# Performance work log

Measured on AMD Instinct MI355X. Metric: run time of the kernel, lower is better.

## Reference

```python
import jax, jax.numpy as jnp
import numpy as np

K = 7
PAD = K // 2
SIG_L = (4.0, 6.0, 8.0)
SIG_S = (1.0, 2.0, 3.0)
DORD = (0, 1, 2)
ANG = (1, 2, 3, 4)
N_INV, N_EQ, N_CP = 8, 16, 16
LN_EPS = 1e-5


def _polar_grid(k):
    c = jnp.arange(k, dtype=jnp.float32) - (k - 1) / 2.0
    gy, gx = jnp.meshgrid(c, c, indexing='ij')
    r = jnp.sqrt(gx * gx + gy * gy + 1e-8)
    th = jnp.arctan2(gy, gx)
    return r, th


def _gaussian_basis(r, sigmas, orders, n):
    # Gaussian-derivative radial basis (Eqs. 13-14): cycle over (order, sigma) combos.
    combos = [(s, d) for d in orders for s in sigmas]
    mats = []
    for i in range(n):
        s, d = combos[i % len(combos)]
        u = r / s
        g = jnp.exp(-0.5 * u * u)
        p = jnp.ones_like(u) if d == 0 else (u if d == 1 else u * u - 1.0)
        psi = p * g
        mats.append(psi / jnp.sqrt(jnp.sum(psi * psi) + 1e-8))
    return jnp.stack(mats)  # [n, K, K]


def _harmonic_basis(r, th, w1, b1, w2, b2, n):
    # Circular harmonics (Eqs. 15-16): learnable radial MLP x cos/sin(n*theta).
    kk = r.size
    rad = jnp.tanh(r.reshape(kk, 1) @ w1 + b1) @ w2 + b2  # [K*K, M]
    tf = th.reshape(kk)
    ang = jnp.stack([f(o * tf) for o in ANG for f in (jnp.cos, jnp.sin)])  # [2L, K*K]
    basis = (rad.T[:, None, :] * ang[None, :, :]).reshape(-1, K, K)  # [M*2L, K, K]
    return basis[:n]


def _coeff(z, w1, b1, w2, b2, n, cout):
    h = jax.nn.relu(z @ w1 + b1)
    return (h @ w2 + b2).reshape(z.shape[0], n, cout)  # [B, N, C_out]


def _pconv(feature, kernel):
    # Per-sample kernel shared across input channels: conv2d with weight
    # expand over C_in == conv of the channel-sum with the per-(b,o) kernel.
    B, Cin, H, W = feature.shape
    Cout = kernel.shape[1]
    fs = feature.sum(axis=1)[None]  # [1, B, H, W]
    rhs = kernel.reshape(B * Cout, 1, K, K)
    out = jax.lax.conv_general_dilated(fs, rhs, (1, 1), [(PAD, PAD), (PAD, PAD)], feature_group_count=B)
    return out.reshape(B, Cout, H, W)


def _ln_c(x, g, b):
    # LayerNorm over channel dim (permute(0,2,3,1) -> LN -> permute back)
    mu = jnp.mean(x, axis=1, keepdims=True)
    var = jnp.var(x, axis=1, keepdims=True)
    return (x - mu) * jax.lax.rsqrt(var + LN_EPS) * g[None, :, None, None] + b[None, :, None, None]


def setup_inputs() -> dict:
    key = jax.random.key(0)
    ks = jax.random.split(key, 16)
    B, C, H, W = 16, 256, 48, 48
    hid = 64
    d = {}
    d['feature'] = jax.random.normal(ks[0], (B, C, H, W), jnp.float32)
    for i, (name, n) in enumerate([('inv', N_INV), ('eq', N_EQ), ('cp', N_CP)]):
        d[f'cg_{name}_w1'] = jax.random.normal(ks[1 + 4 * i], (C, hid), jnp.float32) * 0.05
        d[f'cg_{name}_b1'] = jnp.zeros((hid,), jnp.float32)
        d[f'cg_{name}_w2'] = jax.random.normal(ks[2 + 4 * i], (hid, n * C), jnp.float32) * 0.05
        d[f'cg_{name}_b2'] = jnp.zeros((n * C,), jnp.float32)
    d['rad_w1'] = jax.random.normal(ks[13], (1, 32), jnp.float32)
    d['rad_b1'] = jnp.zeros((32,), jnp.float32)
    d['rad_w2'] = jax.random.normal(ks[14], (32, 2), jnp.float32) * 0.3
    d['rad_b2'] = jnp.zeros((2,), jnp.float32)
    for name in ('inv', 'eq', 'cp'):
        d[f'ln_{name}_g'] = jnp.ones((C,), jnp.float32)
        d[f'ln_{name}_b'] = jnp.zeros((C,), jnp.float32)
    return d


def reference(feature, cg_inv_w1, cg_inv_b1, cg_inv_w2, cg_inv_b2,
              cg_eq_w1, cg_eq_b1, cg_eq_w2, cg_eq_b2,
              cg_cp_w1, cg_cp_b1, cg_cp_w2, cg_cp_b2,
              rad_w1, rad_b1, rad_w2, rad_b2,
              ln_inv_g, ln_inv_b, ln_eq_g, ln_eq_b, ln_cp_g, ln_cp_b):
    C_out = ln_inv_g.shape[0]
    r, th = _polar_grid(K)
    b_inv = _gaussian_basis(r, SIG_L, DORD, N_INV)
    b_eq = _gaussian_basis(r, SIG_S, DORD, N_EQ)
    b_cp = _harmonic_basis(r, th, rad_w1, rad_b1, rad_w2, rad_b2, N_CP)
    z = feature.mean(axis=(2, 3))  # [B, C] global average pool
    # Eq. 12: kernel[b,c] = sum_n coeff[b,n,c] * basis[n]
    k_inv = jnp.einsum('bnc,nhw->bchw', _coeff(z, cg_inv_w1, cg_inv_b1, cg_inv_w2, cg_inv_b2, N_INV, C_out), b_inv)
    k_eq = jnp.einsum('bnc,nhw->bchw', _coeff(z, cg_eq_w1, cg_eq_b1, cg_eq_w2, cg_eq_b2, N_EQ, C_out), b_eq)
    k_cp = jnp.einsum('bnc,nhw->bchw', _coeff(z, cg_cp_w1, cg_cp_b1, cg_cp_w2, cg_cp_b2, N_CP, C_out), b_cp)
    f_inv = _ln_c(_pconv(feature, k_inv), ln_inv_g, ln_inv_b)
    f_eq = _ln_c(_pconv(feature, k_eq), ln_eq_g, ln_eq_b)
    f_cp = _ln_c(_pconv(feature, k_cp), ln_cp_g, ln_cp_b)
    return (f_inv, f_eq, f_cp)
```

## Files before the change

kernel.cpp:

```cpp
#include <hip/hip_runtime.h>

#define B_ 16
#define C_ 256
#define H_ 48
#define W_ 48
#define HW_ 2304

typedef float f4 __attribute__((ext_vector_type(4)));

#define WS_ZPART 0
#define WS_FSPART 36864
#define WS_FSPAD 184320
#define WS_BASIS 232704
#define WS_COEFFT 234784
#define WS_MQ 431392
#define WS_CMEAN 443680
#define WS_H 444448
#define WS_G 447520

__device__ __forceinline__ float wave_sum(float v) {
#pragma unroll
  for (int off = 32; off; off >>= 1) v += __shfl_xor(v, off, 64);
  return v;
}

__global__ __launch_bounds__(256) void zfs1_kernel(const float* __restrict__ feat,
                                                   float* __restrict__ zpart,
                                                   float* __restrict__ fspart) {
  int b = blockIdx.x, cc = blockIdx.y, pc = blockIdx.z;
  int tid = threadIdx.x;
  int p = pc * 256 + tid;
  const float* f = feat + ((size_t)b * C_ + cc * 64) * HW_ + p;
  __shared__ float zsum[256];
  int w = tid >> 6, lane = tid & 63;
  float facc = 0.f;
#pragma unroll 8
  for (int j = 0; j < 64; ++j) {
    float v = f[(size_t)j * HW_];
    facc += v;
    float s = wave_sum(v);
    if (lane == 0) zsum[w * 64 + j] = s;
  }
  fspart[cc * (B_ * HW_) + b * HW_ + p] = facc;
  __syncthreads();
  if (tid < 64) {
    float zv = zsum[tid] + zsum[64 + tid] + zsum[128 + tid] + zsum[192 + tid];
    zpart[((size_t)b * 256 + cc * 64 + tid) * 9 + pc] = zv;
  }
}

__global__ __launch_bounds__(256) void fsfin_kernel(
    const float* __restrict__ fspart, const float* __restrict__ rw1,
    const float* __restrict__ rb1, const float* __restrict__ rw2,
    const float* __restrict__ rb2, float* __restrict__ fspad,
    float* __restrict__ basis) {
  int bx = blockIdx.x, tid = threadIdx.x;
  if (bx < 16) {
    int b = bx;
    for (int i = tid; i < 54 * 56; i += 256) {
      int yy = i / 56;
      int xx = i - yy * 56;
      int y = yy - 3, x = xx - 3;
      float v = 0.f;
      if (y >= 0 && y < H_ && x >= 0 && x < W_) {
        int idx = b * HW_ + y * W_ + x;
        v = fspart[idx] + fspart[B_ * HW_ + idx] + fspart[2 * B_ * HW_ + idx] +
            fspart[3 * B_ * HW_ + idx];
      }
      fspad[b * 3024 + i] = v;
    }
    return;
  }
  if (tid >= 64) return;
  int t = tid;
  float r = 0.f, th = 0.f;
  if (t < 49) {
    int iy = t / 7, ix = t - iy * 7;
    float gy = (float)iy - 3.f, gx = (float)ix - 3.f;
    r = sqrtf(gx * gx + gy * gy + 1e-8f);
    th = atan2f(gy, gx);
  }
  if (bx < 40) {
    int f = bx - 16;
    const float SIGL[3] = {4.f, 6.f, 8.f};
    const float SIGS[3] = {1.f, 2.f, 3.f};
    int i = (f < 8) ? f : f - 8;
    int c = i % 9, d = c / 3;
    float s = (f < 8) ? SIGL[c % 3] : SIGS[c % 3];
    float p = 0.f;
    if (t < 49) {
      float u = r / s;
      float g = expf(-0.5f * u * u);
      p = ((d == 0) ? 1.f : ((d == 1) ? u : (u * u - 1.f))) * g;
    }
    float ss = wave_sum(p * p);
    if (t < 49) basis[f * 52 + t] = p / sqrtf(ss + 1e-8f);
  } else if (t < 49) {
    int i = bx - 40;
    float r0 = rb2[0], r1 = rb2[1];
    for (int j = 0; j < 32; ++j) {
      float h = tanhf(r * rw1[j] + rb1[j]);
      r0 = fmaf(h, rw2[2 * j], r0);
      r1 = fmaf(h, rw2[2 * j + 1], r1);
    }
    int m = i >> 3, a = i & 7, o = (a >> 1) + 1;
    float ang = (a & 1) ? sinf((float)o * th) : cosf((float)o * th);
    basis[(24 + i) * 52 + t] = (m ? r1 : r0) * ang;
  }
}

__global__ __launch_bounds__(256) void gconv_kernel(
    const float* __restrict__ fspad, const float* __restrict__ basis,
    float* __restrict__ G) {
  int tid = threadIdx.x;
  int ng = blockIdx.y;
  int b = blockIdx.x / 9, pc = blockIdx.x - 9 * (blockIdx.x / 9);
  int p = pc * 256 + tid;
  int py = p / 48, px = p - py * 48;
  const float* wb = fspad + b * 3024 + py * 56 + px;
  float wreg[49];
#pragma unroll
  for (int dy = 0; dy < 7; ++dy)
#pragma unroll
    for (int dx = 0; dx < 7; ++dx) wreg[dy * 7 + dx] = wb[dy * 56 + dx];
  float* go = G + ((size_t)b * 40 + ng * 10) * HW_ + p;
#pragma unroll 2
  for (int ni = 0; ni < 10; ++ni) {
    const float* bs = basis + (ng * 10 + ni) * 52;
    float acc = 0.f;
#pragma unroll
    for (int k = 0; k < 49; ++k) acc = fmaf(bs[k], wreg[k], acc);
    go[(size_t)ni * HW_] = acc;
  }
}

__global__ __launch_bounds__(256) void h_kernel(
    const float* __restrict__ zpart, const float* __restrict__ w1i,
    const float* __restrict__ b1i, const float* __restrict__ w1e,
    const float* __restrict__ b1e, const float* __restrict__ w1c,
    const float* __restrict__ b1c, float* __restrict__ hout) {
  int branch = blockIdx.x >> 4, b = blockIdx.x & 15, tid = threadIdx.x;
  const float* w1 = branch == 0 ? w1i : (branch == 1 ? w1e : w1c);
  const float* b1 = branch == 0 ? b1i : (branch == 1 ? b1e : b1c);
  __shared__ float zs[256], hp[256];
  {
    const float* zp = zpart + ((size_t)b * 256 + tid) * 9;
    float za = 0.f;
#pragma unroll
    for (int i = 0; i < 9; ++i) za += zp[i];
    zs[tid] = za * (1.f / (float)HW_);
  }
  __syncthreads();
  int j = tid & 63, part = tid >> 6;
  float acc = 0.f;
  const float* wp = w1 + part * 64 * 64 + j;
#pragma unroll
  for (int q = 0; q < 64; ++q) acc = fmaf(zs[part * 64 + q], wp[q * 64], acc);
  hp[tid] = acc;
  __syncthreads();
  if (tid < 64)
    hout[blockIdx.x * 64 + tid] = fmaxf(
        b1[tid] + hp[tid] + hp[64 + tid] + hp[128 + tid] + hp[192 + tid], 0.f);
}

__global__ __launch_bounds__(256) void coeffA_kernel(
    const float* __restrict__ hbuf, const float* __restrict__ w2i,
    const float* __restrict__ b2i, const float* __restrict__ w2e,
    const float* __restrict__ b2e, const float* __restrict__ w2c,
    const float* __restrict__ b2c, float* __restrict__ coeffT) {
  int b = blockIdx.x, ng = blockIdx.y, c = threadIdx.x;
  int branch = (ng < 8) ? 0 : ((ng < 24) ? 1 : 2);
  int nl = ng - ((branch == 0) ? 0 : ((branch == 1) ? 8 : 24));
  int Nc = (branch == 0) ? 8 : 16;
  const float* w2 = branch == 0 ? w2i : (branch == 1 ? w2e : w2c);
  const float* b2 = branch == 0 ? b2i : (branch == 1 ? b2e : b2c);
  __shared__ float hs[64];
  if (c < 64) hs[c] = hbuf[(branch * 16 + b) * 64 + c];
  __syncthreads();
  float acc = b2[nl * 256 + c];
  const float* wp = w2 + (size_t)nl * 256 + c;
  size_t stride = (size_t)Nc * 256;
#pragma unroll
  for (int jj = 0; jj < 64; ++jj) acc = fmaf(hs[jj], wp[jj * stride], acc);
  float* ctp = coeffT + ((size_t)(b * 3 + branch) * 256 + c) * 16;
  ctp[nl] = acc;
  if (branch == 0) ctp[nl + 8] = 0.f;
}

__global__ __launch_bounds__(256) void mstat_kernel(
    const float* __restrict__ coeffT, float* __restrict__ Mq,
    float* __restrict__ cmean) {
  int b = blockIdx.x, branch = blockIdx.y, tid = threadIdx.x;
  __shared__ float Ls[4096];
  const float* base = coeffT + (size_t)(b * 3 + branch) * 4096;
#pragma unroll
  for (int k = 0; k < 16; ++k) Ls[k * 256 + tid] = base[k * 256 + tid];
  __syncthreads();
  int nn = tid >> 4, mm = tid & 15;
  float dot = 0.f;
#pragma unroll 8
  for (int cc = 0; cc < 256; ++cc)
    dot = fmaf(Ls[((cc & 15) * 16 + (cc >> 4)) * 16 + nn],
               Ls[((cc & 15) * 16 + (cc >> 4)) * 16 + mm], dot);
  Mq[(b * 3 + branch) * 256 + tid] = dot * (1.f / 256.f);
  if (tid < 16) {
    float s = 0.f;
    for (int cc = 0; cc < 256; ++cc) s += Ls[cc * 16 + tid];
    cmean[(b * 3 + branch) * 16 + tid] = s * (1.f / 256.f);
  }
}

__global__ __launch_bounds__(256) void pout_kernel(
    const float* __restrict__ G, const float* __restrict__ coeffT,
    const float* __restrict__ Mq, const float* __restrict__ cmean,
    const float* __restrict__ g0, const float* __restrict__ be0,
    const float* __restrict__ g1, const float* __restrict__ be1,
    const float* __restrict__ g2, const float* __restrict__ be2,
    float* __restrict__ out) {
  int branch = blockIdx.y;
  int bx = blockIdx.x;
  int b = bx / 72, pc = bx - b * 72;
  int p0 = pc * 32;
  int tid = threadIdx.x;
  int n0 = (branch == 0) ? 0 : ((branch == 1) ? 8 : 24);
  __shared__ __align__(16) float Ms[256];
  __shared__ float cms[16];
  __shared__ __align__(16) float smu[32];
  __shared__ __align__(16) float srs[32];
  Ms[tid] = Mq[(b * 3 + branch) * 256 + tid];
  if (tid < 16) cms[tid] = cmean[(b * 3 + branch) * 16 + tid];
  __syncthreads();
  if (tid < 32) {
    int p = p0 + tid;
    float gr[16];
#pragma unroll
    for (int n = 0; n < 16; ++n)
      gr[n] = G[((size_t)b * 40 + n0 + n) * HW_ + p];
    float mu = 0.f, q = 0.f;
#pragma unroll
    for (int n = 0; n < 16; ++n) {
      mu = fmaf(cms[n], gr[n], mu);
      float t = 0.f;
#pragma unroll
      for (int m = 0; m < 16; ++m) t = fmaf(Ms[n * 16 + m], gr[m], t);
      q = fmaf(gr[n], t, q);
    }
    smu[tid] = mu;
    srs[tid] = rsqrtf(q - mu * mu + 1e-5f);
  }
  __syncthreads();
  int pg = tid & 7, cg = tid >> 3;
  int p = p0 + pg * 4;
  f4 Gr[16];
#pragma unroll
  for (int n = 0; n < 16; ++n)
    Gr[n] = *reinterpret_cast<const f4*>(G + ((size_t)b * 40 + n0 + n) * HW_ + p);
  f4 mu4 = *reinterpret_cast<const f4*>(smu + pg * 4);
  f4 rs4 = *reinterpret_cast<const f4*>(srs + pg * 4);
  const float* gp = (branch == 0) ? g0 : ((branch == 1) ? g1 : g2);
  const float* bp = (branch == 0) ? be0 : ((branch == 1) ? be1 : be2);
  int c0 = cg * 8;
  float gch[8], bch[8];
#pragma unroll
  for (int i = 0; i < 8; ++i) {
    gch[i] = gp[c0 + i];
    bch[i] = bp[c0 + i];
  }
  const f4* ct4 =
      reinterpret_cast<const f4*>(coeffT + ((size_t)(b * 3 + branch) * 256 + c0) * 16);
  float* op = out + ((size_t)((branch * 16 + b) * 256 + c0)) * HW_ + p;
#pragma unroll
  for (int ci = 0; ci < 8; ++ci) {
    f4 a = ct4[ci * 4 + 0], bb = ct4[ci * 4 + 1];
    f4 cc = ct4[ci * 4 + 2], dd = ct4[ci * 4 + 3];
    f4 v = a.x * Gr[0];
    v += a.y * Gr[1];
    v += a.z * Gr[2];
    v += a.w * Gr[3];
    v += bb.x * Gr[4];
    v += bb.y * Gr[5];
    v += bb.z * Gr[6];
    v += bb.w * Gr[7];
    v += cc.x * Gr[8];
    v += cc.y * Gr[9];
    v += cc.z * Gr[10];
    v += cc.w * Gr[11];
    v += dd.x * Gr[12];
    v += dd.y * Gr[13];
    v += dd.z * Gr[14];
    v += dd.w * Gr[15];
    f4 o = (v - mu4) * rs4;
    o = o * gch[ci] + bch[ci];
    __builtin_nontemporal_store(o, reinterpret_cast<f4*>(op + (size_t)ci * HW_));
  }
}

extern "C" void kernel_launch(void* const* d_in, const int* in_sizes, int n_in,
                              void* d_out, int out_size, void* d_ws,
                              size_t ws_size, hipStream_t stream) {
  const float* feat = (const float*)d_in[0];
  float* ws = (float*)d_ws;
  float* zpart = ws + WS_ZPART;
  float* fspart = ws + WS_FSPART;
  float* fspad = ws + WS_FSPAD;
  float* basis = ws + WS_BASIS;
  float* coeffT = ws + WS_COEFFT;
  float* Mq = ws + WS_MQ;
  float* cmean = ws + WS_CMEAN;
  float* hbuf = ws + WS_H;
  float* G = ws + WS_G;

  zfs1_kernel<<<dim3(16, 4, 9), 256, 0, stream>>>(feat, zpart, fspart);
  fsfin_kernel<<<56, 256, 0, stream>>>(
      fspart, (const float*)d_in[13], (const float*)d_in[14],
      (const float*)d_in[15], (const float*)d_in[16], fspad, basis);
  gconv_kernel<<<dim3(144, 4), 256, 0, stream>>>(fspad, basis, G);
  h_kernel<<<48, 256, 0, stream>>>(zpart, (const float*)d_in[1],
                                   (const float*)d_in[2], (const float*)d_in[5],
                                   (const float*)d_in[6], (const float*)d_in[9],
                                   (const float*)d_in[10], hbuf);
  coeffA_kernel<<<dim3(16, 40), 256, 0, stream>>>(
      hbuf, (const float*)d_in[3], (const float*)d_in[4],
      (const float*)d_in[7], (const float*)d_in[8], (const float*)d_in[11],
      (const float*)d_in[12], coeffT);
  mstat_kernel<<<dim3(16, 3), 256, 0, stream>>>(coeffT, Mq, cmean);
  pout_kernel<<<dim3(16 * 72, 3), 256, 0, stream>>>(
      G, coeffT, Mq, cmean, (const float*)d_in[17], (const float*)d_in[18],
      (const float*)d_in[19], (const float*)d_in[20], (const float*)d_in[21],
      (const float*)d_in[22], (float*)d_out);
}
```

Before: 268.7 us.

## Merge small prep kernels into two launches and double pixels per output block

Folds the hidden-layer MLP into the padding/basis prep kernel, and the coefficient kernel into the Gaussian-conv kernel, cutting the launch count from seven to five. The merged kernels pick their role from the block index. The output LayerNorm kernel now covers 64 pixels per block in two halves instead of 32, which halves the block count and reuses the per-channel gamma/beta and coefficient loads. Trade-offs are more register pressure in the output kernel and branch-heterogeneous blocks in the merged kernels.

```diff
diff --git a/kernel.cpp b/kernel.cpp
--- a/kernel.cpp
+++ b/kernel.cpp
@@ -49,11 +49,15 @@
   }
 }
 
-__global__ __launch_bounds__(256) void fsfin_kernel(
-    const float* __restrict__ fspart, const float* __restrict__ rw1,
-    const float* __restrict__ rb1, const float* __restrict__ rw2,
-    const float* __restrict__ rb2, float* __restrict__ fspad,
-    float* __restrict__ basis) {
+__global__ __launch_bounds__(256) void prep_kernel(
+    const float* __restrict__ fspart, const float* __restrict__ zpart,
+    const float* __restrict__ rw1, const float* __restrict__ rb1,
+    const float* __restrict__ rw2, const float* __restrict__ rb2,
+    const float* __restrict__ w1i, const float* __restrict__ b1i,
+    const float* __restrict__ w1e, const float* __restrict__ b1e,
+    const float* __restrict__ w1c, const float* __restrict__ b1c,
+    float* __restrict__ fspad, float* __restrict__ basis,
+    float* __restrict__ hout) {
   int bx = blockIdx.x, tid = threadIdx.x;
   if (bx < 16) {
     int b = bx;
@@ -71,50 +75,104 @@
     }
     return;
   }
-  if (tid >= 64) return;
-  int t = tid;
-  float r = 0.f, th = 0.f;
-  if (t < 49) {
-    int iy = t / 7, ix = t - iy * 7;
-    float gy = (float)iy - 3.f, gx = (float)ix - 3.f;
-    r = sqrtf(gx * gx + gy * gy + 1e-8f);
-    th = atan2f(gy, gx);
-  }
-  if (bx < 40) {
-    int f = bx - 16;
-    const float SIGL[3] = {4.f, 6.f, 8.f};
-    const float SIGS[3] = {1.f, 2.f, 3.f};
-    int i = (f < 8) ? f : f - 8;
-    int c = i % 9, d = c / 3;
-    float s = (f < 8) ? SIGL[c % 3] : SIGS[c % 3];
-    float p = 0.f;
+  if (bx < 56) {
+    if (tid >= 64) return;
+    int t = tid;
+    float r = 0.f, th = 0.f;
     if (t < 49) {
-      float u = r / s;
-      float g = expf(-0.5f * u * u);
-      p = ((d == 0) ? 1.f : ((d == 1) ? u : (u * u - 1.f))) * g;
-    }
-    float ss = wave_sum(p * p);
-    if (t < 49) basis[f * 52 + t] = p / sqrtf(ss + 1e-8f);
-  } else if (t < 49) {
-    int i = bx - 40;
-    float r0 = rb2[0], r1 = rb2[1];
-    for (int j = 0; j < 32; ++j) {
-      float h = tanhf(r * rw1[j] + rb1[j]);
-      r0 = fmaf(h, rw2[2 * j], r0);
-      r1 = fmaf(h, rw2[2 * j + 1], r1);
-    }
-    int m = i >> 3, a = i & 7, o = (a >> 1) + 1;
-    float ang = (a & 1) ? sinf((float)o * th) : cosf((float)o * th);
-    basis[(24 + i) * 52 + t] = (m ? r1 : r0) * ang;
-  }
-}
-
-__global__ __launch_bounds__(256) void gconv_kernel(
+      int iy = t / 7, ix = t - iy * 7;
+      float gy = (float)iy - 3.f, gx = (float)ix - 3.f;
+      r = sqrtf(gx * gx + gy * gy + 1e-8f);
+      th = atan2f(gy, gx);
+    }
+    if (bx < 40) {
+      int f = bx - 16;
+      const float SIGL[3] = {4.f, 6.f, 8.f};
+      const float SIGS[3] = {1.f, 2.f, 3.f};
+      int i = (f < 8) ? f : f - 8;
+      int c = i % 9, d = c / 3;
+      float s = (f < 8) ? SIGL[c % 3] : SIGS[c % 3];
+      float p = 0.f;
+      if (t < 49) {
+        float u = r / s;
+        float g = expf(-0.5f * u * u);
+        p = ((d == 0) ? 1.f : ((d == 1) ? u : (u * u - 1.f))) * g;
+      }
+      float ss = wave_sum(p * p);
+      if (t < 49) basis[f * 52 + t] = p / sqrtf(ss + 1e-8f);
+    } else if (t < 49) {
+      int i = bx - 40;
+      float r0 = rb2[0], r1 = rb2[1];
+      for (int j = 0; j < 32; ++j) {
+        float h = tanhf(r * rw1[j] + rb1[j]);
+        r0 = fmaf(h, rw2[2 * j], r0);
+        r1 = fmaf(h, rw2[2 * j + 1], r1);
+      }
+      int m = i >> 3, a = i & 7, o = (a >> 1) + 1;
+      float ang = (a & 1) ? sinf((float)o * th) : cosf((float)o * th);
+      basis[(24 + i) * 52 + t] = (m ? r1 : r0) * ang;
+    }
+    return;
+  }
+  int idx = bx - 56;
+  int branch = idx >> 4, b = idx & 15;
+  const float* w1 = branch == 0 ? w1i : (branch == 1 ? w1e : w1c);
+  const float* b1 = branch == 0 ? b1i : (branch == 1 ? b1e : b1c);
+  __shared__ float zs[256], hp[256];
+  {
+    const float* zp = zpart + ((size_t)b * 256 + tid) * 9;
+    float za = 0.f;
+#pragma unroll
+    for (int i = 0; i < 9; ++i) za += zp[i];
+    zs[tid] = za * (1.f / (float)HW_);
+  }
+  __syncthreads();
+  int j = tid & 63, part = tid >> 6;
+  float acc = 0.f;
+  const float* wp = w1 + part * 64 * 64 + j;
+#pragma unroll
+  for (int q = 0; q < 64; ++q) acc = fmaf(zs[part * 64 + q], wp[q * 64], acc);
+  hp[tid] = acc;
+  __syncthreads();
+  if (tid < 64)
+    hout[idx * 64 + tid] = fmaxf(
+        b1[tid] + hp[tid] + hp[64 + tid] + hp[128 + tid] + hp[192 + tid], 0.f);
+}
+
+__global__ __launch_bounds__(256) void gca_kernel(
     const float* __restrict__ fspad, const float* __restrict__ basis,
-    float* __restrict__ G) {
+    const float* __restrict__ hbuf, const float* __restrict__ w2i,
+    const float* __restrict__ b2i, const float* __restrict__ w2e,
+    const float* __restrict__ b2e, const float* __restrict__ w2c,
+    const float* __restrict__ b2c, float* __restrict__ G,
+    float* __restrict__ coeffT) {
   int tid = threadIdx.x;
-  int ng = blockIdx.y;
-  int b = blockIdx.x / 9, pc = blockIdx.x - 9 * (blockIdx.x / 9);
+  if (blockIdx.x < 640) {
+    int j = blockIdx.x;
+    int b = j / 40, ng = j - b * 40;
+    int c = tid;
+    int branch = (ng < 8) ? 0 : ((ng < 24) ? 1 : 2);
+    int nl = ng - ((branch == 0) ? 0 : ((branch == 1) ? 8 : 24));
+    int Nc = (branch == 0) ? 8 : 16;
+    const float* w2 = branch == 0 ? w2i : (branch == 1 ? w2e : w2c);
+    const float* b2 = branch == 0 ? b2i : (branch == 1 ? b2e : b2c);
+    __shared__ float hs[64];
+    if (c < 64) hs[c] = hbuf[(branch * 16 + b) * 64 + c];
+    __syncthreads();
+    float acc = b2[nl * 256 + c];
+    const float* wp = w2 + (size_t)nl * 256 + c;
+    size_t stride = (size_t)Nc * 256;
+#pragma unroll
+    for (int jj = 0; jj < 64; ++jj) acc = fmaf(hs[jj], wp[jj * stride], acc);
+    float* ctp = coeffT + ((size_t)(b * 3 + branch) * 256 + c) * 16;
+    ctp[nl] = acc;
+    if (branch == 0) ctp[nl + 8] = 0.f;
+    return;
+  }
+  int i = blockIdx.x - 640;
+  int ng = i / 144;
+  int r = i - ng * 144;
+  int b = r / 9, pc = r - b * 9;
   int p = pc * 256 + tid;
   int py = p / 48, px = p - py * 48;
   const float* wb = fspad + b * 3024 + py * 56 + px;
@@ -132,59 +190,6 @@
     for (int k = 0; k < 49; ++k) acc = fmaf(bs[k], wreg[k], acc);
     go[(size_t)ni * HW_] = acc;
   }
-}
-
-__global__ __launch_bounds__(256) void h_kernel(
-    const float* __restrict__ zpart, const float* __restrict__ w1i,
-    const float* __restrict__ b1i, const float* __restrict__ w1e,
-    const float* __restrict__ b1e, const float* __restrict__ w1c,
-    const float* __restrict__ b1c, float* __restrict__ hout) {
-  int branch = blockIdx.x >> 4, b = blockIdx.x & 15, tid = threadIdx.x;
-  const float* w1 = branch == 0 ? w1i : (branch == 1 ? w1e : w1c);
-  const float* b1 = branch == 0 ? b1i : (branch == 1 ? b1e : b1c);
-  __shared__ float zs[256], hp[256];
-  {
-    const float* zp = zpart + ((size_t)b * 256 + tid) * 9;
-    float za = 0.f;
-#pragma unroll
-    for (int i = 0; i < 9; ++i) za += zp[i];
-    zs[tid] = za * (1.f / (float)HW_);
-  }
-  __syncthreads();
-  int j = tid & 63, part = tid >> 6;
-  float acc = 0.f;
-  const float* wp = w1 + part * 64 * 64 + j;
-#pragma unroll
-  for (int q = 0; q < 64; ++q) acc = fmaf(zs[part * 64 + q], wp[q * 64], acc);
-  hp[tid] = acc;
-  __syncthreads();
-  if (tid < 64)
-    hout[blockIdx.x * 64 + tid] = fmaxf(
-        b1[tid] + hp[tid] + hp[64 + tid] + hp[128 + tid] + hp[192 + tid], 0.f);
-}
-
-__global__ __launch_bounds__(256) void coeffA_kernel(
-    const float* __restrict__ hbuf, const float* __restrict__ w2i,
-    const float* __restrict__ b2i, const float* __restrict__ w2e,
-    const float* __restrict__ b2e, const float* __restrict__ w2c,
-    const float* __restrict__ b2c, float* __restrict__ coeffT) {
-  int b = blockIdx.x, ng = blockIdx.y, c = threadIdx.x;
-  int branch = (ng < 8) ? 0 : ((ng < 24) ? 1 : 2);
-  int nl = ng - ((branch == 0) ? 0 : ((branch == 1) ? 8 : 24));
-  int Nc = (branch == 0) ? 8 : 16;
-  const float* w2 = branch == 0 ? w2i : (branch == 1 ? w2e : w2c);
-  const float* b2 = branch == 0 ? b2i : (branch == 1 ? b2e : b2c);
-  __shared__ float hs[64];
-  if (c < 64) hs[c] = hbuf[(branch * 16 + b) * 64 + c];
-  __syncthreads();
-  float acc = b2[nl * 256 + c];
-  const float* wp = w2 + (size_t)nl * 256 + c;
-  size_t stride = (size_t)Nc * 256;
-#pragma unroll
-  for (int jj = 0; jj < 64; ++jj) acc = fmaf(hs[jj], wp[jj * stride], acc);
-  float* ctp = coeffT + ((size_t)(b * 3 + branch) * 256 + c) * 16;
-  ctp[nl] = acc;
-  if (branch == 0) ctp[nl + 8] = 0.f;
 }
 
 __global__ __launch_bounds__(256) void mstat_kernel(
@@ -219,18 +224,18 @@
     float* __restrict__ out) {
   int branch = blockIdx.y;
   int bx = blockIdx.x;
-  int b = bx / 72, pc = bx - b * 72;
-  int p0 = pc * 32;
+  int b = bx / 36, pc = bx - b * 36;
+  int p0 = pc * 64;
   int tid = threadIdx.x;
   int n0 = (branch == 0) ? 0 : ((branch == 1) ? 8 : 24);
   __shared__ __align__(16) float Ms[256];
   __shared__ float cms[16];
-  __shared__ __align__(16) float smu[32];
-  __shared__ __align__(16) float srs[32];
+  __shared__ __align__(16) float smu[64];
+  __shared__ __align__(16) float srs[64];
   Ms[tid] = Mq[(b * 3 + branch) * 256 + tid];
   if (tid < 16) cms[tid] = cmean[(b * 3 + branch) * 16 + tid];
   __syncthreads();
-  if (tid < 32) {
+  if (tid < 64) {
     int p = p0 + tid;
     float gr[16];
 #pragma unroll
@@ -250,16 +255,9 @@
   }
   __syncthreads();
   int pg = tid & 7, cg = tid >> 3;
-  int p = p0 + pg * 4;
-  f4 Gr[16];
-#pragma unroll
-  for (int n = 0; n < 16; ++n)
-    Gr[n] = *reinterpret_cast<const f4*>(G + ((size_t)b * 40 + n0 + n) * HW_ + p);
-  f4 mu4 = *reinterpret_cast<const f4*>(smu + pg * 4);
-  f4 rs4 = *reinterpret_cast<const f4*>(srs + pg * 4);
+  int c0 = cg * 8;
   const float* gp = (branch == 0) ? g0 : ((branch == 1) ? g1 : g2);
   const float* bp = (branch == 0) ? be0 : ((branch == 1) ? be1 : be2);
-  int c0 = cg * 8;
   float gch[8], bch[8];
 #pragma unroll
   for (int i = 0; i < 8; ++i) {
@@ -268,30 +266,42 @@
   }
   const f4* ct4 =
       reinterpret_cast<const f4*>(coeffT + ((size_t)(b * 3 + branch) * 256 + c0) * 16);
-  float* op = out + ((size_t)((branch * 16 + b) * 256 + c0)) * HW_ + p;
-#pragma unroll
-  for (int ci = 0; ci < 8; ++ci) {
-    f4 a = ct4[ci * 4 + 0], bb = ct4[ci * 4 + 1];
-    f4 cc = ct4[ci * 4 + 2], dd = ct4[ci * 4 + 3];
-    f4 v = a.x * Gr[0];
-    v += a.y * Gr[1];
-    v += a.z * Gr[2];
-    v += a.w * Gr[3];
-    v += bb.x * Gr[4];
-    v += bb.y * Gr[5];
-    v += bb.z * Gr[6];
-    v += bb.w * Gr[7];
-    v += cc.x * Gr[8];
-    v += cc.y * Gr[9];
-    v += cc.z * Gr[10];
-    v += cc.w * Gr[11];
-    v += dd.x * Gr[12];
-    v += dd.y * Gr[13];
-    v += dd.z * Gr[14];
-    v += dd.w * Gr[15];
-    f4 o = (v - mu4) * rs4;
-    o = o * gch[ci] + bch[ci];
-    __builtin_nontemporal_store(o, reinterpret_cast<f4*>(op + (size_t)ci * HW_));
+#pragma unroll
+  for (int half = 0; half < 2; ++half) {
+    int p = p0 + half * 32 + pg * 4;
+    f4 Gr[16];
+#pragma unroll
+    for (int n = 0; n < 16; ++n)
+      Gr[n] =
+          *reinterpret_cast<const f4*>(G + ((size_t)b * 40 + n0 + n) * HW_ + p);
+    f4 mu4 = *reinterpret_cast<const f4*>(smu + half * 32 + pg * 4);
+    f4 rs4 = *reinterpret_cast<const f4*>(srs + half * 32 + pg * 4);
+    float* op = out + ((size_t)((branch * 16 + b) * 256 + c0)) * HW_ + p;
+#pragma unroll
+    for (int ci = 0; ci < 8; ++ci) {
+      f4 a = ct4[ci * 4 + 0], bb = ct4[ci * 4 + 1];
+      f4 cc = ct4[ci * 4 + 2], dd = ct4[ci * 4 + 3];
+      f4 v = a.x * Gr[0];
+      v += a.y * Gr[1];
+      v += a.z * Gr[2];
+      v += a.w * Gr[3];
+      v += bb.x * Gr[4];
+      v += bb.y * Gr[5];
+      v += bb.z * Gr[6];
+      v += bb.w * Gr[7];
+      v += cc.x * Gr[8];
+      v += cc.y * Gr[9];
+      v += cc.z * Gr[10];
+      v += cc.w * Gr[11];
+      v += dd.x * Gr[12];
+      v += dd.y * Gr[13];
+      v += dd.z * Gr[14];
+      v += dd.w * Gr[15];
+      f4 o = (v - mu4) * rs4;
+      o = o * gch[ci] + bch[ci];
+      __builtin_nontemporal_store(o,
+                                  reinterpret_cast<f4*>(op + (size_t)ci * HW_));
+    }
   }
 }
 
@@ -311,20 +321,17 @@
   float* G = ws + WS_G;
 
   zfs1_kernel<<<dim3(16, 4, 9), 256, 0, stream>>>(feat, zpart, fspart);
-  fsfin_kernel<<<56, 256, 0, stream>>>(
-      fspart, (const float*)d_in[13], (const float*)d_in[14],
-      (const float*)d_in[15], (const float*)d_in[16], fspad, basis);
-  gconv_kernel<<<dim3(144, 4), 256, 0, stream>>>(fspad, basis, G);
-  h_kernel<<<48, 256, 0, stream>>>(zpart, (const float*)d_in[1],
-                                   (const float*)d_in[2], (const float*)d_in[5],
-                                   (const float*)d_in[6], (const float*)d_in[9],
-                                   (const float*)d_in[10], hbuf);
-  coeffA_kernel<<<dim3(16, 40), 256, 0, stream>>>(
-      hbuf, (const float*)d_in[3], (const float*)d_in[4],
+  prep_kernel<<<104, 256, 0, stream>>>(
+      fspart, zpart, (const float*)d_in[13], (const float*)d_in[14],
+      (const float*)d_in[15], (const float*)d_in[16], (const float*)d_in[1],
+      (const float*)d_in[2], (const float*)d_in[5], (const float*)d_in[6],
+      (const float*)d_in[9], (const float*)d_in[10], fspad, basis, hbuf);
+  gca_kernel<<<1216, 256, 0, stream>>>(
+      fspad, basis, hbuf, (const float*)d_in[3], (const float*)d_in[4],
       (const float*)d_in[7], (const float*)d_in[8], (const float*)d_in[11],
-      (const float*)d_in[12], coeffT);
+      (const float*)d_in[12], G, coeffT);
   mstat_kernel<<<dim3(16, 3), 256, 0, stream>>>(coeffT, Mq, cmean);
-  pout_kernel<<<dim3(16 * 72, 3), 256, 0, stream>>>(
+  pout_kernel<<<dim3(16 * 36, 3), 256, 0, stream>>>(
       G, coeffT, Mq, cmean, (const float*)d_in[17], (const float*)d_in[18],
       (const float*)d_in[19], (const float*)d_in[20], (const float*)d_in[21],
       (const float*)d_in[22], (float*)d_out);
```

Measured after the change: 258.5 us. -3.8%, faster.
